# Kernel optimization log

Measured on AMD Instinct MI355X. Metric: run time of the kernel, lower is better.

The kernel has to match this reference:

```python
import jax, jax.numpy as jnp
import numpy as np

WINDOW_SIZES = (4, 8, 16, 32)


def setup_inputs() -> dict:
    key = jax.random.key(0)
    k1, k2 = jax.random.split(key)
    B, L, D = 128, 1024, 128
    sequence_emb = jax.random.normal(k1, (B, L, D), dtype=jnp.float32)
    mask = jax.random.randint(k2, (B, L), 0, 2, dtype=jnp.int32)
    return {"sequence_emb": sequence_emb, "mask": mask}


def reference(sequence_emb, mask):
    # sequence_emb: (B, L, D); mask: (B, L) int 0/1
    B, L, D = sequence_emb.shape
    m = mask.astype(sequence_emb.dtype)
    masked = sequence_emb * m[..., None]  # (B, L, D)
    # prefix sums with leading zero so window sum = cs[i+w] - cs[i]
    zero_v = jnp.zeros((B, 1, D), dtype=sequence_emb.dtype)
    cs = jnp.concatenate([zero_v, jnp.cumsum(masked, axis=1)], axis=1)  # (B, L+1, D)
    zero_m = jnp.zeros((B, 1), dtype=sequence_emb.dtype)
    cm = jnp.concatenate([zero_m, jnp.cumsum(m, axis=1)], axis=1)  # (B, L+1)
    outs = []
    for w in WINDOW_SIZES:
        if L < w:
            continue
        win_sum = cs[:, w:, :] - cs[:, :-w, :]          # (B, L-w+1, D)
        win_len = jnp.clip(cm[:, w:] - cm[:, :-w], 1.0)  # (B, L-w+1)
        outs.append(win_sum / win_len[..., None])
    return jnp.concatenate(outs, axis=1)  # (B, sum(L-w+1), D)
```

## Files before the change

kernel.cpp:

```cpp
#include <hip/hip_runtime.h>


namespace {
constexpr int kB    = 128;
constexpr int kL    = 1024;
constexpr int kD    = 128;
constexpr int kD4   = kD / 4;
constexpr int TILE  = 64;
constexpr int HALO  = 32;
constexpr int ROWS  = TILE + HALO;
constexpr int ROUT  = 4040;
constexpr int OFF4  = 0;
constexpr int OFF8  = 1021;
constexpr int OFF16 = 2038;
constexpr int OFF32 = 3047;
}

typedef float v4f __attribute__((ext_vector_type(4)));

__device__ __forceinline__ void nt_store(float4* p, const float4& v) {
    v4f x;
    x.x = v.x; x.y = v.y; x.z = v.z; x.w = v.w;
    __builtin_nontemporal_store(x, reinterpret_cast<v4f*>(p));
}

__device__ __forceinline__ void acc4(float4& a, const float4& x) {
    a.x += x.x; a.y += x.y; a.z += x.z; a.w += x.w;
}
__device__ __forceinline__ void slide4(float4& a, const float4& xin, const float4& xout) {
    a.x += xin.x - xout.x; a.y += xin.y - xout.y;
    a.z += xin.z - xout.z; a.w += xin.w - xout.w;
}
__device__ __forceinline__ float4 scale4(const float4& v, float s) {
    return make_float4(v.x * s, v.y * s, v.z * s, v.w * s);
}

__global__ __launch_bounds__(256)
void msse_kernel(const float* __restrict__ emb,
                 const int*   __restrict__ mask,
                 float*       __restrict__ out) {
    __shared__ float4 s_data[ROWS * kD4];
    __shared__ float  s_mask[ROWS];
    __shared__ float  s_inv[4][TILE];

    const int b  = blockIdx.y;
    const int i0 = blockIdx.x * TILE;
    const int t  = threadIdx.x;

    const float4* gsrc = reinterpret_cast<const float4*>(emb) + (size_t)b * kL * kD4;
    #pragma unroll
    for (int k = 0; k < (ROWS * kD4) / 256; ++k) {
        const int f    = t + k * 256;
        const int row  = f >> 5;
        const int grow = i0 + row;
        float4 v = make_float4(0.f, 0.f, 0.f, 0.f);
        float  m = 0.f;
        if (grow < kL) {
            m = (float)mask[b * kL + grow];
            v = gsrc[(size_t)grow * kD4 + (f & 31)];
            v.x *= m; v.y *= m; v.z *= m; v.w *= m;
        }
        s_data[f] = v;
        if ((f & 31) == 0) s_mask[row] = m;
    }
    __syncthreads();

    if (t < TILE) {
        float c = 0.f, c4 = 0.f, c8 = 0.f, c16 = 0.f;
        #pragma unroll
        for (int j = 0; j < 32; ++j) {
            c += s_mask[t + j];
            if (j == 3)  c4  = c;
            if (j == 7)  c8  = c;
            if (j == 15) c16 = c;
        }
        s_inv[0][t] = 1.f / fmaxf(c4,  1.f);
        s_inv[1][t] = 1.f / fmaxf(c8,  1.f);
        s_inv[2][t] = 1.f / fmaxf(c16, 1.f);
        s_inv[3][t] = 1.f / fmaxf(c,   1.f);
    }
    __syncthreads();

    const int lane  = t & 31;
    const int strip = t >> 5;
    const int base  = strip * 8;

    const float4* col = s_data + lane;

    float4 s4, s8, s16, s32;
    {
        float4 a  = make_float4(0.f, 0.f, 0.f, 0.f);
        float4 t4 = a, t8 = a, t16 = a;
        #pragma unroll
        for (int j = 0; j < 32; ++j) {
            acc4(a, col[(base + j) * kD4]);
            if (j == 3)  t4  = a;
            if (j == 7)  t8  = a;
            if (j == 15) t16 = a;
        }
        s4 = t4; s8 = t8; s16 = t16; s32 = a;
    }

    float4* outb = reinterpret_cast<float4*>(out) + (size_t)b * ROUT * kD4 + lane;

    #pragma unroll
    for (int p = 0; p < 8; ++p) {
        const int il = base + p;
        const int i  = i0 + il;

        if (i <= kL - 4)  nt_store(outb + (size_t)(OFF4  + i) * kD4, scale4(s4,  s_inv[0][il]));
        if (i <= kL - 8)  nt_store(outb + (size_t)(OFF8  + i) * kD4, scale4(s8,  s_inv[1][il]));
        if (i <= kL - 16) nt_store(outb + (size_t)(OFF16 + i) * kD4, scale4(s16, s_inv[2][il]));
        if (i <= kL - 32) nt_store(outb + (size_t)(OFF32 + i) * kD4, scale4(s32, s_inv[3][il]));

        const float4 x0 = col[(il)      * kD4];
        const float4 xa = col[(il + 4)  * kD4];
        const float4 xb = col[(il + 8)  * kD4];
        const float4 xc = col[(il + 16) * kD4];
        const float4 xd = col[(il + 32) * kD4];
        slide4(s4,  xa, x0);
        slide4(s8,  xb, x0);
        slide4(s16, xc, x0);
        slide4(s32, xd, x0);
    }
}

extern "C" void kernel_launch(void* const* d_in, const int* in_sizes, int n_in,
                              void* d_out, int out_size, void* d_ws, size_t ws_size,
                              hipStream_t stream) {
    const float* emb  = (const float*)d_in[0];
    const int*   mask = (const int*)d_in[1];
    float*       out  = (float*)d_out;

    dim3 grid((kL + TILE - 1) / TILE, kB);
    dim3 block(256);
    msse_kernel<<<grid, block, 0, stream>>>(emb, mask, out);
}
```

Baseline: 307.9 us.

## Process two 64-row sub-tiles per block with register prefetch into a shared ring buffer

Each block now covers 128 positions instead of 64, reusing a 96-row shared ring buffer. The next 64 rows are prefetched into registers during the first sub-tile's compute and stores, then written into the ring slots the first sub-tile has finished with. This cuts halo re-reads from 50% to 25% and overlaps global loads with output stores. The cost is more registers per thread, an extra barrier pair, and ring-index arithmetic on shared-memory reads.

```diff
diff --git a/kernel.cpp b/kernel.cpp
--- a/kernel.cpp
+++ b/kernel.cpp
@@ -6,9 +6,9 @@
 constexpr int kL    = 1024;
 constexpr int kD    = 128;
 constexpr int kD4   = kD / 4;
-constexpr int TILE  = 64;
+constexpr int BPOS  = 128;
 constexpr int HALO  = 32;
-constexpr int ROWS  = TILE + HALO;
+constexpr int RING  = 64 + HALO;
 constexpr int ROUT  = 4040;
 constexpr int OFF4  = 0;
 constexpr int OFF8  = 1021;
@@ -23,6 +23,7 @@
     x.x = v.x; x.y = v.y; x.z = v.z; x.w = v.w;
     __builtin_nontemporal_store(x, reinterpret_cast<v4f*>(p));
 }
+__device__ __forceinline__ float4 f4zero() { return make_float4(0.f, 0.f, 0.f, 0.f); }
 
 __device__ __forceinline__ void acc4(float4& a, const float4& x) {
     a.x += x.x; a.y += x.y; a.z += x.z; a.w += x.w;
@@ -39,37 +40,52 @@
 void msse_kernel(const float* __restrict__ emb,
                  const int*   __restrict__ mask,
                  float*       __restrict__ out) {
-    __shared__ float4 s_data[ROWS * kD4];
-    __shared__ float  s_mask[ROWS];
-    __shared__ float  s_inv[4][TILE];
+    __shared__ float4 s_data[RING * kD4];
+    __shared__ float  s_maskf[BPOS + HALO];
+    __shared__ float  s_inv[4][BPOS];
 
     const int b  = blockIdx.y;
-    const int i0 = blockIdx.x * TILE;
+    const int P0 = blockIdx.x * BPOS;
     const int t  = threadIdx.x;
 
     const float4* gsrc = reinterpret_cast<const float4*>(emb) + (size_t)b * kL * kD4;
+
+    if (t < BPOS + HALO) {
+        const int row = P0 + t;
+        s_maskf[t] = (row < kL) ? (float)mask[b * kL + row] : 0.f;
+    }
+
     #pragma unroll
-    for (int k = 0; k < (ROWS * kD4) / 256; ++k) {
+    for (int k = 0; k < (RING * kD4) / 256; ++k) {
         const int f    = t + k * 256;
         const int row  = f >> 5;
-        const int grow = i0 + row;
-        float4 v = make_float4(0.f, 0.f, 0.f, 0.f);
-        float  m = 0.f;
-        if (grow < kL) {
-            m = (float)mask[b * kL + grow];
-            v = gsrc[(size_t)grow * kD4 + (f & 31)];
-            v.x *= m; v.y *= m; v.z *= m; v.w *= m;
-        }
+        const int grow = P0 + row;
+        const float m  = (float)mask[b * kL + grow];
+        float4 v = gsrc[(size_t)grow * kD4 + (f & 31)];
+        v.x *= m; v.y *= m; v.z *= m; v.w *= m;
         s_data[f] = v;
-        if ((f & 31) == 0) s_mask[row] = m;
-    }
-    __syncthreads();
-
-    if (t < TILE) {
+    }
+    __syncthreads();
+
+    float4 pf0, pf1, pf2, pf3, pf4, pf5, pf6, pf7;
+    {
+        const int f  = t;
+        #define PF(K, DST)                                                        \
+        {                                                                         \
+            const int ff   = f + (K) * 256;                                       \
+            const int grow = P0 + 96 + (ff >> 5);                                 \
+            DST = (grow < kL) ? gsrc[(size_t)grow * kD4 + (ff & 31)] : f4zero();  \
+        }
+        PF(0, pf0) PF(1, pf1) PF(2, pf2) PF(3, pf3)
+        PF(4, pf4) PF(5, pf5) PF(6, pf6) PF(7, pf7)
+        #undef PF
+    }
+
+    if (t < BPOS) {
         float c = 0.f, c4 = 0.f, c8 = 0.f, c16 = 0.f;
         #pragma unroll
         for (int j = 0; j < 32; ++j) {
-            c += s_mask[t + j];
+            c += s_maskf[t + j];
             if (j == 3)  c4  = c;
             if (j == 7)  c8  = c;
             if (j == 15) c16 = c;
@@ -83,45 +99,95 @@
 
     const int lane  = t & 31;
     const int strip = t >> 5;
-    const int base  = strip * 8;
-
     const float4* col = s_data + lane;
-
-    float4 s4, s8, s16, s32;
-    {
-        float4 a  = make_float4(0.f, 0.f, 0.f, 0.f);
-        float4 t4 = a, t8 = a, t16 = a;
+    float4* outb = reinterpret_cast<float4*>(out) + (size_t)b * ROUT * kD4 + lane;
+
+    {
+        const int base = strip * 8;
+        float4 s4, s8, s16, s32;
+        {
+            float4 a = f4zero(), t4 = a, t8 = a, t16 = a;
+            #pragma unroll
+            for (int j = 0; j < 32; ++j) {
+                acc4(a, col[(base + j) * kD4]);
+                if (j == 3)  t4  = a;
+                if (j == 7)  t8  = a;
+                if (j == 15) t16 = a;
+            }
+            s4 = t4; s8 = t8; s16 = t16; s32 = a;
+        }
         #pragma unroll
-        for (int j = 0; j < 32; ++j) {
-            acc4(a, col[(base + j) * kD4]);
-            if (j == 3)  t4  = a;
-            if (j == 7)  t8  = a;
-            if (j == 15) t16 = a;
-        }
-        s4 = t4; s8 = t8; s16 = t16; s32 = a;
-    }
-
-    float4* outb = reinterpret_cast<float4*>(out) + (size_t)b * ROUT * kD4 + lane;
-
-    #pragma unroll
-    for (int p = 0; p < 8; ++p) {
-        const int il = base + p;
-        const int i  = i0 + il;
-
-        if (i <= kL - 4)  nt_store(outb + (size_t)(OFF4  + i) * kD4, scale4(s4,  s_inv[0][il]));
-        if (i <= kL - 8)  nt_store(outb + (size_t)(OFF8  + i) * kD4, scale4(s8,  s_inv[1][il]));
-        if (i <= kL - 16) nt_store(outb + (size_t)(OFF16 + i) * kD4, scale4(s16, s_inv[2][il]));
-        if (i <= kL - 32) nt_store(outb + (size_t)(OFF32 + i) * kD4, scale4(s32, s_inv[3][il]));
-
-        const float4 x0 = col[(il)      * kD4];
-        const float4 xa = col[(il + 4)  * kD4];
-        const float4 xb = col[(il + 8)  * kD4];
-        const float4 xc = col[(il + 16) * kD4];
-        const float4 xd = col[(il + 32) * kD4];
-        slide4(s4,  xa, x0);
-        slide4(s8,  xb, x0);
-        slide4(s16, xc, x0);
-        slide4(s32, xd, x0);
+        for (int p = 0; p < 8; ++p) {
+            const int il = base + p;
+            const int i  = P0 + il;
+            nt_store(outb + (size_t)(OFF4  + i) * kD4, scale4(s4,  s_inv[0][il]));
+            nt_store(outb + (size_t)(OFF8  + i) * kD4, scale4(s8,  s_inv[1][il]));
+            nt_store(outb + (size_t)(OFF16 + i) * kD4, scale4(s16, s_inv[2][il]));
+            nt_store(outb + (size_t)(OFF32 + i) * kD4, scale4(s32, s_inv[3][il]));
+            const float4 x0 = col[(il)      * kD4];
+            const float4 xa = col[(il + 4)  * kD4];
+            const float4 xb = col[(il + 8)  * kD4];
+            const float4 xc = col[(il + 16) * kD4];
+            const float4 xd = col[(il + 32) * kD4];
+            slide4(s4,  xa, x0);
+            slide4(s8,  xb, x0);
+            slide4(s16, xc, x0);
+            slide4(s32, xd, x0);
+        }
+    }
+    __syncthreads();
+
+    {
+        #define WR(K, SRC)                                                \
+        {                                                                 \
+            const int ff = t + (K) * 256;                                 \
+            const float m = s_maskf[96 + (ff >> 5)];                      \
+            float4 v = SRC;                                               \
+            v.x *= m; v.y *= m; v.z *= m; v.w *= m;                       \
+            s_data[ff] = v;                                               \
+        }
+        WR(0, pf0) WR(1, pf1) WR(2, pf2) WR(3, pf3)
+        WR(4, pf4) WR(5, pf5) WR(6, pf6) WR(7, pf7)
+        #undef WR
+    }
+    __syncthreads();
+
+    {
+        const int base = 64 + strip * 8;
+        auto ldrow = [&](int r) -> const float4& {
+            const int sl = (r >= RING) ? (r - RING) : r;
+            return col[sl * kD4];
+        };
+        float4 s4, s8, s16, s32;
+        {
+            float4 a = f4zero(), t4 = a, t8 = a, t16 = a;
+            #pragma unroll
+            for (int j = 0; j < 32; ++j) {
+                acc4(a, ldrow(base + j));
+                if (j == 3)  t4  = a;
+                if (j == 7)  t8  = a;
+                if (j == 15) t16 = a;
+            }
+            s4 = t4; s8 = t8; s16 = t16; s32 = a;
+        }
+        #pragma unroll
+        for (int p = 0; p < 8; ++p) {
+            const int il = base + p;
+            const int i  = P0 + il;
+            if (i <= kL - 4)  nt_store(outb + (size_t)(OFF4  + i) * kD4, scale4(s4,  s_inv[0][il]));
+            if (i <= kL - 8)  nt_store(outb + (size_t)(OFF8  + i) * kD4, scale4(s8,  s_inv[1][il]));
+            if (i <= kL - 16) nt_store(outb + (size_t)(OFF16 + i) * kD4, scale4(s16, s_inv[2][il]));
+            if (i <= kL - 32) nt_store(outb + (size_t)(OFF32 + i) * kD4, scale4(s32, s_inv[3][il]));
+            const float4 x0 = ldrow(il);
+            const float4 xa = ldrow(il + 4);
+            const float4 xb = ldrow(il + 8);
+            const float4 xc = ldrow(il + 16);
+            const float4 xd = ldrow(il + 32);
+            slide4(s4,  xa, x0);
+            slide4(s8,  xb, x0);
+            slide4(s16, xc, x0);
+            slide4(s32, xd, x0);
+        }
     }
 }
 
@@ -132,7 +198,7 @@
     const int*   mask = (const int*)d_in[1];
     float*       out  = (float*)d_out;
 
-    dim3 grid((kL + TILE - 1) / TILE, kB);
+    dim3 grid(kL / BPOS, kB);
     dim3 block(256);
     msse_kernel<<<grid, block, 0, stream>>>(emb, mask, out);
 }
```

New measurement: 314.2 us. 1.02x slower.
